# Optimization experiments

Measured on AMD Instinct MI355X. Metric: run time of the kernel, lower is better.

## Reference

```python
import jax, jax.numpy as jnp
import numpy as np

# Mamba2 config fixed by the wrapper: state=32, expand=1, n_groups=1, conv kernel=4
H, P, N, K = 32, 64, 32, 4          # heads, head_dim, state_size, conv kernel
D_MODEL = H * P                      # hidden = intermediate (expand=1) = 2048
CONV_DIM = D_MODEL + 2 * N           # intermediate + 2*n_groups*state = 2112
PROJ = D_MODEL + CONV_DIM + H        # in_proj width = 4192
EPS = 1e-6


def setup_inputs() -> dict:
    key = jax.random.key(0)
    ks = jax.random.split(key, 8)
    B, L = 4, 2048
    w = lambda k, shape, sc=0.02: jax.random.normal(k, shape, jnp.float32) * sc
    return {
        "x": jax.random.normal(ks[0], (B, L, D_MODEL), jnp.float32),
        "W_in": w(ks[1], (D_MODEL, PROJ)),
        "b_in": jnp.zeros((PROJ,), jnp.float32),
        "conv_w": w(ks[2], (CONV_DIM, K), 0.25),
        "conv_b": jnp.zeros((CONV_DIM,), jnp.float32),
        "A_log": jnp.log(jnp.arange(1, H + 1, dtype=jnp.float32)),
        "dt_bias": jax.random.uniform(ks[3], (H,), jnp.float32, -4.0, 0.0),
        "D_param": jnp.ones((H,), jnp.float32),
        "norm_w": jnp.ones((D_MODEL,), jnp.float32),
        "W_out": w(ks[4], (D_MODEL, D_MODEL)),
    }


def reference(x, W_in, b_in, conv_w, conv_b, A_log, dt_bias, D_param, norm_w, W_out):
    B, L, _ = x.shape
    proj = x @ W_in + b_in                                   # (B,L,PROJ)
    gate, hBC, dt_raw = jnp.split(proj, [D_MODEL, D_MODEL + CONV_DIM], axis=-1)

    # causal depthwise conv1d over time (kernel K, left pad K-1), then SiLU
    hp = jnp.pad(hBC, ((0, 0), (K - 1, 0), (0, 0)))
    conv = conv_b + sum(hp[:, k:k + L, :] * conv_w[:, k] for k in range(K))
    conv = jax.nn.silu(conv)

    xs, Bm, Cm = jnp.split(conv, [D_MODEL, D_MODEL + N], axis=-1)
    xs = xs.reshape(B, L, H, P)                              # (B,L,H,P)

    A = -jnp.exp(A_log)                                      # (H,)
    dt = jax.nn.softplus(dt_raw + dt_bias)                   # (B,L,H)
    dA = jnp.exp(dt * A)                                     # (B,L,H)

    def step(hstate, inp):
        dA_t, dt_t, x_t, B_t, C_t = inp                      # (B,H),(B,H),(B,H,P),(B,N),(B,N)
        upd = (dt_t[:, :, None] * x_t)[..., None] * B_t[:, None, None, :]
        hstate = dA_t[:, :, None, None] * hstate + upd       # (B,H,P,N)
        y_t = jnp.einsum('bhpn,bn->bhp', hstate, C_t)
        return hstate, y_t

    h0 = jnp.zeros((B, H, P, N), x.dtype)
    scan_in = (dA.transpose(1, 0, 2), dt.transpose(1, 0, 2),
               xs.transpose(1, 0, 2, 3), Bm.transpose(1, 0, 2), Cm.transpose(1, 0, 2))
    _, ys = jax.lax.scan(step, h0, scan_in)                  # ys: (L,B,H,P)

    y = ys.transpose(1, 0, 2, 3) + D_param[None, None, :, None] * xs
    y = y.reshape(B, L, D_MODEL)

    # gated RMSNorm: gate applied before normalization (MambaRMSNormGated)
    y = y * jax.nn.silu(gate)
    var = jnp.mean(jnp.square(y), axis=-1, keepdims=True)
    y = y * jax.lax.rsqrt(var + EPS) * norm_w
    return y @ W_out
```

## Files before the change

kernel.cpp:

```cpp
#include <hip/hip_runtime.h>
#include <cstdint>
#include <cstddef>

constexpr int kB    = 4;
constexpr int kL    = 2048;
constexpr int kH    = 32;
constexpr int kP    = 64;
constexpr int kN    = 32;
constexpr int kD    = 2048;
constexpr int kProjW = 4192;
constexpr int kLdp  = 4224;
constexpr int kM    = kB * kL;
constexpr int kK    = kD;
constexpr int kLC   = 128;
constexpr int kNC   = kL / kLC;

typedef _Float16 f16x8 __attribute__((ext_vector_type(8)));
typedef float f32x4 __attribute__((ext_vector_type(4)));

__device__ __forceinline__ float lane_bcast(float v, int lane) {
    return __int_as_float(__builtin_amdgcn_readlane(__float_as_int(v), lane));
}
__device__ __forceinline__ float silu_f(float x) { return x / (1.f + __expf(-x)); }

__device__ __forceinline__ void async_copy16(const void* g, void* lds) {
    __builtin_amdgcn_global_load_lds(
        (const __attribute__((address_space(1))) unsigned int*)(uintptr_t)g,
        (__attribute__((address_space(3))) unsigned int*)(uintptr_t)lds,
        16, 0, 0);
}

__global__ __launch_bounds__(256) void cast_f16_kernel(const float* __restrict__ in,
                                                       _Float16* __restrict__ out) {
    size_t i = ((size_t)blockIdx.x * 256 + threadIdx.x) * 8;
    float4 a = *(const float4*)(in + i);
    float4 b = *(const float4*)(in + i + 4);
    f16x8 o;
    o[0] = (_Float16)a.x; o[1] = (_Float16)a.y; o[2] = (_Float16)a.z; o[3] = (_Float16)a.w;
    o[4] = (_Float16)b.x; o[5] = (_Float16)b.y; o[6] = (_Float16)b.z; o[7] = (_Float16)b.w;
    *(f16x8*)(out + i) = o;
}

__global__ __launch_bounds__(256) void transpose_cast_kernel(const float* __restrict__ W,
                                                             _Float16* __restrict__ Wt,
                                                             int R, int C) {
    __shared__ float tile[32][33];
    const int c0 = blockIdx.x * 32;
    const int r0 = blockIdx.y * 32;
    const int tx = threadIdx.x & 31;
    const int ty = threadIdx.x >> 5;
    #pragma unroll
    for (int i = 0; i < 32; i += 8) {
        int rr = r0 + ty + i;
        int cc = c0 + tx;
        tile[ty + i][tx] = (cc < C) ? W[(size_t)rr * C + cc] : 0.f;
    }
    __syncthreads();
    #pragma unroll
    for (int i = 0; i < 32; i += 8) {
        int cc = c0 + ty + i;
        int rr = r0 + tx;
        Wt[(size_t)cc * R + rr] = (_Float16)tile[tx][ty + i];
    }
}

template <bool OUT_F16>
__global__ __launch_bounds__(256, 2) void gemm_bt_kernel(
    const _Float16* __restrict__ A, const _Float16* __restrict__ Bt,
    const float* __restrict__ bias, int nbias,
    void* __restrict__ Cout, int K, int ldc, float* __restrict__ dtside)
{
    __shared__ __attribute__((aligned(16))) _Float16 As[3][256 * 32];
    __shared__ __attribute__((aligned(16))) _Float16 Bs[3][128 * 32];

    const int tid = threadIdx.x;
    const int w   = tid >> 6;
    const int l   = tid & 63;
    const int r   = l & 15;
    const int q   = l >> 4;

    const int pid = blockIdx.x;
    const int i0  = pid >> 3;
    const int m_idx = (pid & 7) * 4 + (i0 & 3);
    const int n_idx = i0 >> 2;

    const size_t tileM = (size_t)m_idx * 256;
    const size_t tileN = (size_t)n_idx * 128;

    const _Float16* gA[4];
    #pragma unroll
    for (int g = 0; g < 4; ++g)
        gA[g] = A + (tileM + (size_t)((w + g * 4) * 16 + r)) * K + q * 8;
    const _Float16* gB[2];
    #pragma unroll
    for (int g = 0; g < 2; ++g)
        gB[g] = Bt + (tileN + (size_t)((w + g * 4) * 16 + r)) * K + q * 8;

    auto stage = [&](int s, int koff) {
        #pragma unroll
        for (int g = 0; g < 4; ++g)
            async_copy16(gA[g] + koff, &As[s][(w + g * 4) * 512]);
        #pragma unroll
        for (int g = 0; g < 2; ++g)
            async_copy16(gB[g] + koff, &Bs[s][(w + g * 4) * 512]);
    };

    const int T = K >> 5;
    stage(0, 0);
    stage(1, 32);

    f32x4 acc[4][8] = {};
    int cs = 0;

    for (int k = 0; k < T; ++k) {
        if (k + 1 < T) asm volatile("s_waitcnt vmcnt(6)" ::: "memory");
        else           asm volatile("s_waitcnt vmcnt(0)" ::: "memory");
        asm volatile("s_barrier" ::: "memory");
        if (k + 2 < T) {
            int ns = cs + 2; if (ns >= 3) ns -= 3;
            stage(ns, (k + 2) * 32);
        }
        f16x8 af[4], bf[8];
        #pragma unroll
        for (int i = 0; i < 4; ++i)
            af[i] = *(const f16x8*)&As[cs][(w * 4 + i) * 512 + l * 8];
        #pragma unroll
        for (int j = 0; j < 8; ++j)
            bf[j] = *(const f16x8*)&Bs[cs][j * 512 + l * 8];
        #pragma unroll
        for (int i = 0; i < 4; ++i)
            #pragma unroll
            for (int j = 0; j < 8; ++j)
                acc[i][j] = __builtin_amdgcn_mfma_f32_16x16x32_f16(af[i], bf[j], acc[i][j], 0, 0, 0);
        cs = (cs + 1 >= 3) ? 0 : cs + 1;
    }

    #pragma unroll
    for (int j = 0; j < 8; ++j) {
        const int col = (int)tileN + j * 16 + r;
        float bv = 0.f;
        if (bias != nullptr && col < nbias) bv = bias[col];
        #pragma unroll
        for (int i = 0; i < 4; ++i) {
            const size_t row = tileM + (size_t)(w * 64 + i * 16 + q * 4);
            #pragma unroll
            for (int u = 0; u < 4; ++u) {
                float v = acc[i][j][u] + bv;
                if (OUT_F16) ((_Float16*)Cout)[(row + u) * ldc + col] = (_Float16)v;
                else         ((float*)Cout)[(row + u) * ldc + col] = v;
                if (dtside != nullptr && col >= 4160 && col < 4192)
                    dtside[(row + u) * 32 + (col - 4160)] = v;
            }
        }
    }
}

__global__ __launch_bounds__(256) void dt_da_kernel(
    const float* __restrict__ dtraw, const float* __restrict__ A_log,
    const float* __restrict__ dt_bias, float* __restrict__ dtv, float* __restrict__ dAv)
{
    int idx = blockIdx.x * 256 + threadIdx.x;
    int t  = idx & (kL - 1);
    int bh = idx >> 11;
    int h  = bh & (kH - 1);
    int b  = bh >> 5;
    float z  = dtraw[((size_t)(b * kL + t)) * kH + h] + dt_bias[h];
    float dt = (z > 20.f) ? z : log1pf(expf(z));
    float dA = expf(dt * -expf(A_log[h]));
    dtv[idx] = dt;
    dAv[idx] = dA;
}

__global__ __launch_bounds__(64) void scan_pass1_kernel(
    const _Float16* __restrict__ projh, const float* __restrict__ conv_w,
    const float* __restrict__ conv_b, const float* __restrict__ dtv,
    const float* __restrict__ dAv, float* __restrict__ cstate, float* __restrict__ Pch)
{
    const int blk = blockIdx.x;
    const int c   = blk & (kNC - 1);
    const int bh  = blk >> 4;
    const int h   = bh & (kH - 1);
    const int b   = bh >> 5;
    const int l   = threadIdx.x;
    const int t0  = c * kLC;

    const int chx = h * kP + l;
    const int chb = 2048 + (l & 31);
    const float xw0 = conv_w[chx*4+0], xw1 = conv_w[chx*4+1], xw2 = conv_w[chx*4+2], xw3 = conv_w[chx*4+3];
    const float xbb = conv_b[chx];
    const float bw0 = conv_w[chb*4+0], bw1 = conv_w[chb*4+1], bw2 = conv_w[chb*4+2], bw3 = conv_w[chb*4+3];
    const float bbb = conv_b[chb];

    const _Float16* pb = projh + (size_t)b * kL * kLdp;
    const int colx = 2048 + chx;
    const int colb = 2048 + chb;

    float xq0=0.f, xq1=0.f, xq2=0.f, bq0=0.f, bq1=0.f, bq2=0.f;
    if (c > 0) {
        xq0 = (float)pb[(size_t)(t0-3)*kLdp + colx];
        xq1 = (float)pb[(size_t)(t0-2)*kLdp + colx];
        xq2 = (float)pb[(size_t)(t0-1)*kLdp + colx];
        bq0 = (float)pb[(size_t)(t0-3)*kLdp + colb];
        bq1 = (float)pb[(size_t)(t0-2)*kLdp + colb];
        bq2 = (float)pb[(size_t)(t0-1)*kLdp + colb];
    }

    float hs[kN];
    #pragma unroll
    for (int n = 0; n < kN; ++n) hs[n] = 0.f;
    float Pp = 1.f;
    const float* dtp = dtv + (size_t)bh * kL;
    const float* dAp = dAv + (size_t)bh * kL;

    #pragma unroll 1
    for (int t = t0; t < t0 + kLC; ++t) {
        const size_t ro = (size_t)t * kLdp;
        float xv = (float)pb[ro + colx];
        float bv = (float)pb[ro + colb];
        float sx = silu_f(xbb + xw0*xq0 + xw1*xq1 + xw2*xq2 + xw3*xv);
        float sb = silu_f(bbb + bw0*bq0 + bw1*bq1 + bw2*bq2 + bw3*bv);
        xq0=xq1; xq1=xq2; xq2=xv;
        bq0=bq1; bq1=bq2; bq2=bv;
        float dt = dtp[t], dA = dAp[t];
        float dtx = dt * sx;
        Pp *= dA;
        #pragma unroll
        for (int n = 0; n < kN; ++n)
            hs[n] = fmaf(dA, hs[n], dtx * lane_bcast(sb, n));
    }
    float* cs = cstate + (size_t)blk * (kP * kN) + l * kN;
    #pragma unroll
    for (int n = 0; n < kN; ++n) cs[n] = hs[n];
    if (l == 0) Pch[blk] = Pp;
}

__global__ __launch_bounds__(256) void scan_pass2_kernel(float* __restrict__ cstate,
                                                         const float* __restrict__ Pch) {
    const int bh  = blockIdx.x;
    const int off = threadIdx.x * 8;
    float s[8];
    #pragma unroll
    for (int i = 0; i < 8; ++i) s[i] = 0.f;
    float* base = cstate + (size_t)bh * (kNC * kP * kN) + off;
    #pragma unroll 1
    for (int c = 0; c < kNC; ++c) {
        float* cs = base + c * (kP * kN);
        float Pp = Pch[bh * kNC + c];
        #pragma unroll
        for (int i = 0; i < 8; ++i) {
            float loc = cs[i];
            cs[i] = s[i];
            s[i] = fmaf(Pp, s[i], loc);
        }
    }
}

__global__ __launch_bounds__(64) void scan_pass3_kernel(
    const _Float16* __restrict__ projh, const float* __restrict__ conv_w,
    const float* __restrict__ conv_b, const float* __restrict__ dtv,
    const float* __restrict__ dAv, const float* __restrict__ cstate,
    const float* __restrict__ D_param, float* __restrict__ ypre)
{
    const int blk = blockIdx.x;
    const int c   = blk & (kNC - 1);
    const int bh  = blk >> 4;
    const int h   = bh & (kH - 1);
    const int b   = bh >> 5;
    const int l   = threadIdx.x;
    const int t0  = c * kLC;

    const int chx = h * kP + l;
    const int chc = 2048 + l;
    const float xw0 = conv_w[chx*4+0], xw1 = conv_w[chx*4+1], xw2 = conv_w[chx*4+2], xw3 = conv_w[chx*4+3];
    const float xbb = conv_b[chx];
    const float cw0 = conv_w[chc*4+0], cw1 = conv_w[chc*4+1], cw2 = conv_w[chc*4+2], cw3 = conv_w[chc*4+3];
    const float cbb = conv_b[chc];

    const _Float16* pb = projh + (size_t)b * kL * kLdp;
    const int colx = 2048 + chx;
    const int colc = 2048 + chc;

    float xq0=0.f, xq1=0.f, xq2=0.f, cq0=0.f, cq1=0.f, cq2=0.f;
    if (c > 0) {
        xq0 = (float)pb[(size_t)(t0-3)*kLdp + colx];
        xq1 = (float)pb[(size_t)(t0-2)*kLdp + colx];
        xq2 = (float)pb[(size_t)(t0-1)*kLdp + colx];
        cq0 = (float)pb[(size_t)(t0-3)*kLdp + colc];
        cq1 = (float)pb[(size_t)(t0-2)*kLdp + colc];
        cq2 = (float)pb[(size_t)(t0-1)*kLdp + colc];
    }

    float hs[kN];
    const float* cs = cstate + (size_t)blk * (kP * kN) + l * kN;
    #pragma unroll
    for (int n = 0; n < kN; ++n) hs[n] = cs[n];
    const float Dh = D_param[h];
    const float* dtp = dtv + (size_t)bh * kL;
    const float* dAp = dAv + (size_t)bh * kL;
    float* yo = ypre + (size_t)b * kL * kD + h * kP + l;

    #pragma unroll 1
    for (int t = t0; t < t0 + kLC; ++t) {
        const size_t ro = (size_t)t * kLdp;
        float xv = (float)pb[ro + colx];
        float cv = (float)pb[ro + colc];
        float sx = silu_f(xbb + xw0*xq0 + xw1*xq1 + xw2*xq2 + xw3*xv);
        float sc = silu_f(cbb + cw0*cq0 + cw1*cq1 + cw2*cq2 + cw3*cv);
        xq0=xq1; xq1=xq2; xq2=xv;
        cq0=cq1; cq1=cq2; cq2=cv;
        float dt = dtp[t], dA = dAp[t];
        float dtx = dt * sx;
        float y0 = Dh * sx, y1 = 0.f;
        #pragma unroll
        for (int n = 0; n < kN; ++n) {
            float bn = lane_bcast(sc, n);
            float cn = lane_bcast(sc, n + 32);
            hs[n] = fmaf(dA, hs[n], dtx * bn);
            if (n & 1) y1 = fmaf(hs[n], cn, y1);
            else       y0 = fmaf(hs[n], cn, y0);
        }
        yo[(size_t)t * kD] = y0 + y1;
    }
}

__global__ __launch_bounds__(256) void gated_norm_kernel(
    const float* __restrict__ ypre, const _Float16* __restrict__ projh,
    const float* __restrict__ norm_w, _Float16* __restrict__ yh)
{
    const int row = blockIdx.x;
    const int tid = threadIdx.x;
    const float* yr = ypre + (size_t)row * kD;
    const _Float16* gr = projh + (size_t)row * kLdp;
    float v[8];
    float ss = 0.f;
    #pragma unroll
    for (int u = 0; u < 8; ++u) {
        int col = tid + u * 256;
        float g = (float)gr[col];
        float t = yr[col] * (g / (1.f + __expf(-g)));
        v[u] = t;
        ss = fmaf(t, t, ss);
    }
    #pragma unroll
    for (int off = 32; off > 0; off >>= 1) ss += __shfl_xor(ss, off, 64);
    __shared__ float red[4];
    if ((tid & 63) == 0) red[tid >> 6] = ss;
    __syncthreads();
    float tot = (red[0] + red[1]) + (red[2] + red[3]);
    float scl = rsqrtf(tot * (1.f / (float)kD) + 1e-6f);
    #pragma unroll
    for (int u = 0; u < 8; ++u) {
        int col = tid + u * 256;
        yh[(size_t)row * kD + col] = (_Float16)(v[u] * scl * norm_w[col]);
    }
}

extern "C" void kernel_launch(void* const* d_in, const int* in_sizes, int n_in,
                              void* d_out, int out_size, void* d_ws, size_t ws_size,
                              hipStream_t stream)
{
    (void)in_sizes; (void)n_in; (void)out_size; (void)ws_size;
    const float* x       = (const float*)d_in[0];
    const float* W_in    = (const float*)d_in[1];
    const float* b_in    = (const float*)d_in[2];
    const float* conv_w  = (const float*)d_in[3];
    const float* conv_b  = (const float*)d_in[4];
    const float* A_log   = (const float*)d_in[5];
    const float* dt_bias = (const float*)d_in[6];
    const float* D_param = (const float*)d_in[7];
    const float* norm_w  = (const float*)d_in[8];
    const float* W_out   = (const float*)d_in[9];
    float* out = (float*)d_out;

    char* p = (char*)d_ws;
    _Float16* projh = (_Float16*)p; p += (size_t)kM * kLdp * 2;
    _Float16* xh    = (_Float16*)p; p += (size_t)kM * kD * 2;
    _Float16* Wt    = (_Float16*)p; p += (size_t)kLdp * kK * 2;
    _Float16* Wot   = (_Float16*)p; p += (size_t)kD * kK * 2;
    float* dtraw    = (float*)p;    p += (size_t)kM * kH * 4;
    float* dtv      = (float*)p;    p += (size_t)kB * kH * kL * 4;
    float* dAv      = (float*)p;    p += (size_t)kB * kH * kL * 4;
    float* cstate   = (float*)p;    p += (size_t)kB * kH * kNC * kP * kN * 4;
    float* Pch      = (float*)p;    p += (size_t)kB * kH * kNC * 4;
    _Float16* yh = xh;
    float* ypre = out;

    cast_f16_kernel<<<(kM * kD) / (256 * 8), 256, 0, stream>>>(x, xh);
    transpose_cast_kernel<<<dim3(kLdp / 32, kK / 32), 256, 0, stream>>>(W_in, Wt, kK, kProjW);
    transpose_cast_kernel<<<dim3(kD / 32, kK / 32), 256, 0, stream>>>(W_out, Wot, kK, kD);
    gemm_bt_kernel<true><<<(kM / 256) * (kLdp / 128), 256, 0, stream>>>(
        xh, Wt, b_in, kProjW, (void*)projh, kK, kLdp, dtraw);
    dt_da_kernel<<<(kB * kH * kL) / 256, 256, 0, stream>>>(dtraw, A_log, dt_bias, dtv, dAv);
    scan_pass1_kernel<<<kB * kH * kNC, 64, 0, stream>>>(projh, conv_w, conv_b, dtv, dAv, cstate, Pch);
    scan_pass2_kernel<<<kB * kH, 256, 0, stream>>>(cstate, Pch);
    scan_pass3_kernel<<<kB * kH * kNC, 64, 0, stream>>>(projh, conv_w, conv_b, dtv, dAv, cstate, D_param, ypre);
    gated_norm_kernel<<<kM, 256, 0, stream>>>(ypre, projh, norm_w, yh);
    gemm_bt_kernel<false><<<(kM / 256) * (kD / 128), 256, 0, stream>>>(
        yh, Wot, nullptr, 0, (void*)out, kK, kD, nullptr);
}
```

Before: 734.5 us.

## Replace GEMM with 256x256-tile, 8-wave ping-pong pipelined MFMA kernel

Both projections now use a new GEMM kernel with 256x256 output tiles and 512 threads (8 waves in a 2x4 grid), K-step 64, and a double-buffered LDS split into four quarter-tiles. Each quarter is refilled while the waves compute on the others, with barriers and setprio around the MFMA bursts. Workgroups are remapped across XCDs, and the in_proj weight is padded to 4352 columns with a column-validity guard in the epilogue. The goal is more operand reuse per LDS load and better overlap of loads with MFMA work. The cost is 128 KB of LDS, a large accumulator count per thread, and some wasted work on the padded columns.

```diff
diff --git a/kernel.cpp b/kernel.cpp
--- a/kernel.cpp
+++ b/kernel.cpp
@@ -10,6 +10,7 @@
 constexpr int kD    = 2048;
 constexpr int kProjW = 4192;
 constexpr int kLdp  = 4224;
+constexpr int kNp1  = 4352;
 constexpr int kM    = kB * kL;
 constexpr int kK    = kD;
 constexpr int kLC   = 128;
@@ -65,89 +66,158 @@
 }
 
 template <bool OUT_F16>
-__global__ __launch_bounds__(256, 2) void gemm_bt_kernel(
+__global__ __launch_bounds__(512, 2) void gemm256_kernel(
     const _Float16* __restrict__ A, const _Float16* __restrict__ Bt,
     const float* __restrict__ bias, int nbias,
-    void* __restrict__ Cout, int K, int ldc, float* __restrict__ dtside)
-{
-    __shared__ __attribute__((aligned(16))) _Float16 As[3][256 * 32];
-    __shared__ __attribute__((aligned(16))) _Float16 Bs[3][128 * 32];
+    void* __restrict__ Cout, int K, int ldc, int nvalid, int nn,
+    float* __restrict__ dtside)
+{
+    __shared__ __attribute__((aligned(16))) _Float16 lds[2 * 4 * 8192];
 
     const int tid = threadIdx.x;
-    const int w   = tid >> 6;
-    const int l   = tid & 63;
-    const int r   = l & 15;
-    const int q   = l >> 4;
-
+    const int l = tid & 63, r = l & 15, q = l >> 4;
+    const int w = tid >> 6, wm = w >> 2, wn = w & 3;
+
+    const int nwg = gridDim.x;
+    const int q8 = nwg >> 3;
     const int pid = blockIdx.x;
-    const int i0  = pid >> 3;
-    const int m_idx = (pid & 7) * 4 + (i0 & 3);
-    const int n_idx = i0 >> 2;
-
+    const int wg = (pid & 7) * q8 + (pid >> 3);
+    const int m_idx = wg / nn;
+    const int n_idx = wg - m_idx * nn;
     const size_t tileM = (size_t)m_idx * 256;
-    const size_t tileN = (size_t)n_idx * 128;
-
-    const _Float16* gA[4];
-    #pragma unroll
-    for (int g = 0; g < 4; ++g)
-        gA[g] = A + (tileM + (size_t)((w + g * 4) * 16 + r)) * K + q * 8;
-    const _Float16* gB[2];
-    #pragma unroll
-    for (int g = 0; g < 2; ++g)
-        gB[g] = Bt + (tileN + (size_t)((w + g * 4) * 16 + r)) * K + q * 8;
-
-    auto stage = [&](int s, int koff) {
-        #pragma unroll
-        for (int g = 0; g < 4; ++g)
-            async_copy16(gA[g] + koff, &As[s][(w + g * 4) * 512]);
-        #pragma unroll
-        for (int g = 0; g < 2; ++g)
-            async_copy16(gB[g] + koff, &Bs[s][(w + g * 4) * 512]);
+    const size_t tileN = (size_t)n_idx * 256;
+
+    const int sR = ((tid >> 7) << 4) | (tid & 15);
+    const int sC = ((tid >> 4) & 7) << 3;
+    const _Float16* aSrc = A  + (tileM + sR) * (size_t)K + sC;
+    const _Float16* bSrc = Bt + (tileN + sR) * (size_t)K + sC;
+    _Float16* dst0 = lds + tid * 8;
+
+    auto STAGE = [&](int buf, int part, const _Float16* src, int half, int kt2) {
+        const _Float16* s = src + (size_t)(half * 128) * K + kt2 * 64;
+        _Float16* d = dst0 + buf * 32768 + part * 8192;
+        async_copy16(s, d);
+        async_copy16(s + (size_t)64 * K, d + 4096);
     };
 
-    const int T = K >> 5;
-    stage(0, 0);
-    stage(1, 32);
-
-    f32x4 acc[4][8] = {};
-    int cs = 0;
-
-    for (int k = 0; k < T; ++k) {
-        if (k + 1 < T) asm volatile("s_waitcnt vmcnt(6)" ::: "memory");
-        else           asm volatile("s_waitcnt vmcnt(0)" ::: "memory");
-        asm volatile("s_barrier" ::: "memory");
-        if (k + 2 < T) {
-            int ns = cs + 2; if (ns >= 3) ns -= 3;
-            stage(ns, (k + 2) * 32);
-        }
-        f16x8 af[4], bf[8];
-        #pragma unroll
-        for (int i = 0; i < 4; ++i)
-            af[i] = *(const f16x8*)&As[cs][(w * 4 + i) * 512 + l * 8];
-        #pragma unroll
-        for (int j = 0; j < 8; ++j)
-            bf[j] = *(const f16x8*)&Bs[cs][j * 512 + l * 8];
+    const int NT = K >> 6;
+    STAGE(0, 0, aSrc, 0, 0); STAGE(0, 3, bSrc, 1, 0);
+    STAGE(0, 1, aSrc, 1, 0); STAGE(0, 2, bSrc, 0, 0);
+    STAGE(1, 0, aSrc, 0, 1); STAGE(1, 3, bSrc, 1, 1);
+    STAGE(1, 1, aSrc, 1, 1);
+    asm volatile("s_waitcnt vmcnt(6)" ::: "memory");
+    asm volatile("s_barrier" ::: "memory");
+
+    f32x4 acc[8][4] = {};
+    f16x8 afr[4][2], bfr[2][2], bfr2[2][2];
+
+    const int aRd = wm * 4 * 2048 + l * 16;
+    const int bRd = wn * 2 * 2048 + l * 16;
+
+    for (int kt = 0; kt < NT; ++kt) {
+        const int bsel = kt & 1;
+        const char* base = (const char*)lds + bsel * 65536;
+
+        #pragma unroll
+        for (int i = 0; i < 4; ++i) {
+            afr[i][0] = *(const f16x8*)(base + 0 * 16384 + aRd + i * 2048);
+            afr[i][1] = *(const f16x8*)(base + 0 * 16384 + aRd + i * 2048 + 1024);
+        }
+        #pragma unroll
+        for (int j = 0; j < 2; ++j) {
+            bfr[j][0] = *(const f16x8*)(base + 2 * 16384 + bRd + j * 2048);
+            bfr[j][1] = *(const f16x8*)(base + 2 * 16384 + bRd + j * 2048 + 1024);
+        }
+        if (kt + 1 < NT) STAGE(bsel ^ 1, 2, bSrc, 0, kt + 1);
+        asm volatile("s_barrier" ::: "memory");
+        asm volatile("s_waitcnt lgkmcnt(0)" ::: "memory");
+        __builtin_amdgcn_s_setprio(1);
         #pragma unroll
         for (int i = 0; i < 4; ++i)
             #pragma unroll
-            for (int j = 0; j < 8; ++j)
-                acc[i][j] = __builtin_amdgcn_mfma_f32_16x16x32_f16(af[i], bf[j], acc[i][j], 0, 0, 0);
-        cs = (cs + 1 >= 3) ? 0 : cs + 1;
-    }
-
-    #pragma unroll
-    for (int j = 0; j < 8; ++j) {
-        const int col = (int)tileN + j * 16 + r;
+            for (int j = 0; j < 2; ++j) {
+                acc[i][j] = __builtin_amdgcn_mfma_f32_16x16x32_f16(afr[i][0], bfr[j][0], acc[i][j], 0, 0, 0);
+                acc[i][j] = __builtin_amdgcn_mfma_f32_16x16x32_f16(afr[i][1], bfr[j][1], acc[i][j], 0, 0, 0);
+            }
+        __builtin_amdgcn_s_setprio(0);
+        asm volatile("s_barrier" ::: "memory");
+
+        #pragma unroll
+        for (int j = 0; j < 2; ++j) {
+            bfr2[j][0] = *(const f16x8*)(base + 3 * 16384 + bRd + j * 2048);
+            bfr2[j][1] = *(const f16x8*)(base + 3 * 16384 + bRd + j * 2048 + 1024);
+        }
+        if (kt + 2 < NT) STAGE(bsel, 0, aSrc, 0, kt + 2);
+        asm volatile("s_barrier" ::: "memory");
+        asm volatile("s_waitcnt lgkmcnt(0)" ::: "memory");
+        __builtin_amdgcn_s_setprio(1);
+        #pragma unroll
+        for (int i = 0; i < 4; ++i)
+            #pragma unroll
+            for (int j = 0; j < 2; ++j) {
+                acc[i][2 + j] = __builtin_amdgcn_mfma_f32_16x16x32_f16(afr[i][0], bfr2[j][0], acc[i][2 + j], 0, 0, 0);
+                acc[i][2 + j] = __builtin_amdgcn_mfma_f32_16x16x32_f16(afr[i][1], bfr2[j][1], acc[i][2 + j], 0, 0, 0);
+            }
+        __builtin_amdgcn_s_setprio(0);
+        asm volatile("s_barrier" ::: "memory");
+
+        #pragma unroll
+        for (int i = 0; i < 4; ++i) {
+            afr[i][0] = *(const f16x8*)(base + 1 * 16384 + aRd + i * 2048);
+            afr[i][1] = *(const f16x8*)(base + 1 * 16384 + aRd + i * 2048 + 1024);
+        }
+        if (kt + 2 < NT) STAGE(bsel, 3, bSrc, 1, kt + 2);
+        asm volatile("s_barrier" ::: "memory");
+        asm volatile("s_waitcnt lgkmcnt(0)" ::: "memory");
+        __builtin_amdgcn_s_setprio(1);
+        #pragma unroll
+        for (int i = 0; i < 4; ++i)
+            #pragma unroll
+            for (int j = 0; j < 2; ++j) {
+                acc[4 + i][2 + j] = __builtin_amdgcn_mfma_f32_16x16x32_f16(afr[i][0], bfr2[j][0], acc[4 + i][2 + j], 0, 0, 0);
+                acc[4 + i][2 + j] = __builtin_amdgcn_mfma_f32_16x16x32_f16(afr[i][1], bfr2[j][1], acc[4 + i][2 + j], 0, 0, 0);
+            }
+        __builtin_amdgcn_s_setprio(0);
+        asm volatile("s_barrier" ::: "memory");
+
+        #pragma unroll
+        for (int j = 0; j < 2; ++j) {
+            bfr[j][0] = *(const f16x8*)(base + 2 * 16384 + bRd + j * 2048);
+            bfr[j][1] = *(const f16x8*)(base + 2 * 16384 + bRd + j * 2048 + 1024);
+        }
+        if (kt + 2 < NT) STAGE(bsel, 1, aSrc, 1, kt + 2);
+        asm volatile("s_barrier" ::: "memory");
+        asm volatile("s_waitcnt lgkmcnt(0)" ::: "memory");
+        __builtin_amdgcn_s_setprio(1);
+        #pragma unroll
+        for (int i = 0; i < 4; ++i)
+            #pragma unroll
+            for (int j = 0; j < 2; ++j) {
+                acc[4 + i][j] = __builtin_amdgcn_mfma_f32_16x16x32_f16(afr[i][0], bfr[j][0], acc[4 + i][j], 0, 0, 0);
+                acc[4 + i][j] = __builtin_amdgcn_mfma_f32_16x16x32_f16(afr[i][1], bfr[j][1], acc[4 + i][j], 0, 0, 0);
+            }
+        __builtin_amdgcn_s_setprio(0);
+        if (kt + 2 < NT) asm volatile("s_waitcnt vmcnt(6)" ::: "memory");
+        else             asm volatile("s_waitcnt vmcnt(0)" ::: "memory");
+        asm volatile("s_barrier" ::: "memory");
+    }
+
+    #pragma unroll
+    for (int bb = 0; bb < 4; ++bb) {
+        const int nh = bb >> 1, j = bb & 1;
+        const int col = (int)tileN + nh * 128 + wn * 32 + j * 16 + r;
+        if (col >= nvalid) continue;
         float bv = 0.f;
         if (bias != nullptr && col < nbias) bv = bias[col];
         #pragma unroll
-        for (int i = 0; i < 4; ++i) {
-            const size_t row = tileM + (size_t)(w * 64 + i * 16 + q * 4);
+        for (int aa = 0; aa < 8; ++aa) {
+            const int mh = aa >> 2, i = aa & 3;
+            const size_t row = tileM + (size_t)(mh * 128 + wm * 64 + i * 16 + q * 4);
             #pragma unroll
             for (int u = 0; u < 4; ++u) {
-                float v = acc[i][j][u] + bv;
-                if (OUT_F16) ((_Float16*)Cout)[(row + u) * ldc + col] = (_Float16)v;
-                else         ((float*)Cout)[(row + u) * ldc + col] = v;
+                float v = acc[aa][bb][u] + bv;
+                if (OUT_F16) ((_Float16*)Cout)[(row + u) * (size_t)ldc + col] = (_Float16)v;
+                else         ((float*)Cout)[(row + u) * (size_t)ldc + col] = v;
                 if (dtside != nullptr && col >= 4160 && col < 4192)
                     dtside[(row + u) * 32 + (col - 4160)] = v;
             }
@@ -375,7 +445,7 @@
     char* p = (char*)d_ws;
     _Float16* projh = (_Float16*)p; p += (size_t)kM * kLdp * 2;
     _Float16* xh    = (_Float16*)p; p += (size_t)kM * kD * 2;
-    _Float16* Wt    = (_Float16*)p; p += (size_t)kLdp * kK * 2;
+    _Float16* Wt    = (_Float16*)p; p += (size_t)kNp1 * kK * 2;
     _Float16* Wot   = (_Float16*)p; p += (size_t)kD * kK * 2;
     float* dtraw    = (float*)p;    p += (size_t)kM * kH * 4;
     float* dtv      = (float*)p;    p += (size_t)kB * kH * kL * 4;
@@ -386,15 +456,15 @@
     float* ypre = out;
 
     cast_f16_kernel<<<(kM * kD) / (256 * 8), 256, 0, stream>>>(x, xh);
-    transpose_cast_kernel<<<dim3(kLdp / 32, kK / 32), 256, 0, stream>>>(W_in, Wt, kK, kProjW);
+    transpose_cast_kernel<<<dim3(kNp1 / 32, kK / 32), 256, 0, stream>>>(W_in, Wt, kK, kProjW);
     transpose_cast_kernel<<<dim3(kD / 32, kK / 32), 256, 0, stream>>>(W_out, Wot, kK, kD);
-    gemm_bt_kernel<true><<<(kM / 256) * (kLdp / 128), 256, 0, stream>>>(
-        xh, Wt, b_in, kProjW, (void*)projh, kK, kLdp, dtraw);
+    gemm256_kernel<true><<<(kM / 256) * (kNp1 / 256), 512, 0, stream>>>(
+        xh, Wt, b_in, kProjW, (void*)projh, kK, kLdp, kLdp, kNp1 / 256, dtraw);
     dt_da_kernel<<<(kB * kH * kL) / 256, 256, 0, stream>>>(dtraw, A_log, dt_bias, dtv, dAv);
     scan_pass1_kernel<<<kB * kH * kNC, 64, 0, stream>>>(projh, conv_w, conv_b, dtv, dAv, cstate, Pch);
     scan_pass2_kernel<<<kB * kH, 256, 0, stream>>>(cstate, Pch);
     scan_pass3_kernel<<<kB * kH * kNC, 64, 0, stream>>>(projh, conv_w, conv_b, dtv, dAv, cstate, D_param, ypre);
     gated_norm_kernel<<<kM, 256, 0, stream>>>(ypre, projh, norm_w, yh);
-    gemm_bt_kernel<false><<<(kM / 256) * (kD / 128), 256, 0, stream>>>(
-        yh, Wot, nullptr, 0, (void*)out, kK, kD, nullptr);
-}
+    gemm256_kernel<false><<<(kM / 256) * (kD / 256), 512, 0, stream>>>(
+        yh, Wot, nullptr, 0, (void*)out, kK, kD, kD, kD / 256, nullptr);
+}
```

Measured after the change: 686.7 us. 6.5% less time.
